# Kernel optimization log

Hardware: AMD Instinct MI355X
Metric: run time of the kernel (lower is better)

The kernel has to match this reference:

```python
import jax, jax.numpy as jnp
import numpy as np

D_MODEL = 1024
N_HEADS = 16
THRESHOLD = 0.8


def setup_inputs() -> dict:
    key = jax.random.key(0)
    ks = jax.random.split(key, 12)
    B, L, D = 2, 2048, D_MODEL
    s = 1.0 / np.sqrt(D)
    return {
        "q_x": jax.random.normal(ks[0], (B, L, D), jnp.float32),
        "k_x": jax.random.normal(ks[1], (B, L, D), jnp.float32),
        "v_x": jax.random.normal(ks[2], (B, L, D), jnp.float32),
        "energy": jax.random.normal(ks[3], (B, L, D), jnp.float32),
        "Wq": jax.random.normal(ks[4], (D, D), jnp.float32) * s,
        "bq": jnp.zeros((D,), jnp.float32),
        "Wk": jax.random.normal(ks[5], (D, D), jnp.float32) * s,
        "bk": jnp.zeros((D,), jnp.float32),
        "Wv": jax.random.normal(ks[6], (D, D), jnp.float32) * s,
        "bv": jnp.zeros((D,), jnp.float32),
        "Wo": jax.random.normal(ks[7], (D, D), jnp.float32) * s,
        "bo": jnp.zeros((D,), jnp.float32),
    }


def reference(q_x, k_x, v_x, energy, Wq, bq, Wk, bk, Wv, bv, Wo, bo):
    B, L, D = q_x.shape
    H = N_HEADS
    Dh = D // H
    # projections -> (B, H, L, Dh)
    Q = (q_x @ Wq + bq).reshape(B, L, H, Dh).transpose(0, 2, 1, 3)
    K = (k_x @ Wk + bk).reshape(B, -1, H, Dh).transpose(0, 2, 1, 3)
    V = (v_x @ Wv + bv).reshape(B, -1, H, Dh).transpose(0, 2, 1, 3)
    sc = jnp.einsum("bhqd,bhkd->bhqk", Q, K) / jnp.sqrt(jnp.float32(Dh))
    # energy mask: (B, Lk) -> broadcast over heads/queries
    mask = jnp.mean(jnp.abs(energy), axis=-1) > THRESHOLD  # (B, Lk)
    sc = jnp.where(mask[:, None, None, :], sc, -jnp.inf)
    w = jnp.nan_to_num(jax.nn.softmax(sc, axis=-1), nan=0.0)
    o = jnp.einsum("bhqk,bhkd->bhqd", w, V).transpose(0, 2, 1, 3).reshape(B, L, D)
    return o @ Wo + bo
```

## Files before the change

### kernel.cpp

```cpp
#include <hip/hip_runtime.h>
#include <hip/hip_bf16.h>
#include <cstdint>

#define DEVI static __device__ __forceinline__

typedef __attribute__((ext_vector_type(8))) short s16x8;
typedef __attribute__((ext_vector_type(4))) float f32x4;
typedef __attribute__((ext_vector_type(2))) unsigned int u32x2;

DEVI unsigned short f2bf(float f) {
  union { float f; unsigned int u; } v; v.f = f;
  return (unsigned short)((v.u + 0x7FFFu + ((v.u >> 16) & 1u)) >> 16);
}

DEVI unsigned int pk2bf(float a, float b) {
  __hip_bfloat162 h2 = __float22bfloat162_rn(float2{a, b});
  return *(unsigned int*)&h2;
}

DEVI void g2l16(const void* g, void* l) {
  __builtin_amdgcn_global_load_lds((const __attribute__((address_space(1))) void*)g,
                                   (__attribute__((address_space(3))) void*)l, 16, 0, 0);
}

__global__ __launch_bounds__(256) void prep_kernel(const float* __restrict__ a,
                                                   const float* __restrict__ b,
                                                   const float* __restrict__ c,
                                                   const float* __restrict__ energy,
                                                   unsigned short* __restrict__ oa,
                                                   unsigned short* __restrict__ ob,
                                                   unsigned short* __restrict__ oc,
                                                   int* __restrict__ flags,
                                                   const float* __restrict__ W0,
                                                   const float* __restrict__ W1,
                                                   const float* __restrict__ W2,
                                                   const float* __restrict__ W3,
                                                   unsigned short* __restrict__ T0,
                                                   unsigned short* __restrict__ T1,
                                                   unsigned short* __restrict__ T2,
                                                   unsigned short* __restrict__ T3) {
  const int gid = blockIdx.x;
  const int t = threadIdx.x;
  __shared__ float lds[64][65];
  if (gid < 6144) {
    const float* in = gid < 2048 ? a : gid < 4096 ? b : c;
    unsigned short* out = gid < 2048 ? oa : gid < 4096 ? ob : oc;
    const int blk = gid & 2047;
    int i = (blk * 256 + t) * 8;
    f32x4 x = *(const f32x4*)(in + i);
    f32x4 y = *(const f32x4*)(in + i + 4);
    s16x8 o;
    o[0] = (short)f2bf(x[0]); o[1] = (short)f2bf(x[1]);
    o[2] = (short)f2bf(x[2]); o[3] = (short)f2bf(x[3]);
    o[4] = (short)f2bf(y[0]); o[5] = (short)f2bf(y[1]);
    o[6] = (short)f2bf(y[2]); o[7] = (short)f2bf(y[3]);
    *(s16x8*)(out + i) = o;
    return;
  }
  if (gid < 10240) {
    const int row = gid - 6144;
    f32x4 v = *(const f32x4*)(energy + (size_t)row * 1024 + t * 4);
    float s = fabsf(v[0]) + fabsf(v[1]) + fabsf(v[2]) + fabsf(v[3]);
#pragma unroll
    for (int off = 1; off < 64; off <<= 1) s += __shfl_xor(s, off);
    if ((t & 63) == 0) lds[0][t >> 6] = s;
    __syncthreads();
    if (t == 0) {
      float tot = lds[0][0] + lds[0][1] + lds[0][2] + lds[0][3];
      flags[row] = (tot * (1.0f / 1024.0f) > 0.8f) ? 1 : 0;
    }
    return;
  }
  const int x = gid - 10240;
  const int z = x >> 8, rem = x & 255;
  const float* W = z == 0 ? W0 : z == 1 ? W1 : z == 2 ? W2 : W3;
  unsigned short* WT = z == 0 ? T0 : z == 1 ? T1 : z == 2 ? T2 : T3;
  const int n0 = (rem >> 4) * 64, k0 = (rem & 15) * 64;
#pragma unroll
  for (int p = 0; p < 4; p++) {
    int r = p * 16 + (t >> 4);
    int cc = (t & 15) * 4;
    f32x4 v = *(const f32x4*)(W + (size_t)(k0 + r) * 1024 + n0 + cc);
    lds[r][cc] = v[0]; lds[r][cc + 1] = v[1]; lds[r][cc + 2] = v[2]; lds[r][cc + 3] = v[3];
  }
  __syncthreads();
  const int cc = t >> 2, gk = t & 3;
#pragma unroll
  for (int hv = 0; hv < 2; hv++) {
    s16x8 o;
#pragma unroll
    for (int j = 0; j < 8; j++) o[j] = (short)f2bf(lds[gk * 16 + hv * 8 + j][cc]);
    *(s16x8*)(WT + (size_t)(n0 + cc) * 1024 + k0 + gk * 16 + hv * 8) = o;
  }
}

__global__ __launch_bounds__(256) void scan_kernel(const int* __restrict__ flags,
                                                   int* __restrict__ inv,
                                                   int* __restrict__ cnt) {
  const int b = blockIdx.x, t = threadIdx.x;
  const int* f = flags + b * 2048;
  int* iv = inv + b * 2048;
#pragma unroll
  for (int j = 0; j < 8; j++) iv[t * 8 + j] = 0;
  int loc[8], s = 0;
#pragma unroll
  for (int j = 0; j < 8; j++) { loc[j] = f[t * 8 + j]; s += loc[j]; }
  const int lane = t & 63, w = t >> 6;
  int ps = s;
#pragma unroll
  for (int off = 1; off < 64; off <<= 1) {
    int o = __shfl_up(ps, off);
    if (lane >= off) ps += o;
  }
  __shared__ int wsum[4];
  if (lane == 63) wsum[w] = ps;
  __syncthreads();
  int woff = 0;
  for (int i = 0; i < w; i++) woff += wsum[i];
  int excl = woff + ps - s;
#pragma unroll
  for (int j = 0; j < 8; j++) {
    if (loc[j]) { iv[excl] = t * 8 + j; excl++; }
  }
  if (t == 255) cnt[b] = woff + ps;
}


__global__ __launch_bounds__(256, 8) void proj_qkv(const unsigned short* __restrict__ xq,
                                                   const unsigned short* __restrict__ xk,
                                                   const unsigned short* __restrict__ xv,
                                                   const unsigned short* __restrict__ WTq,
                                                   const unsigned short* __restrict__ WTk,
                                                   const unsigned short* __restrict__ WTv,
                                                   const float* __restrict__ bq,
                                                   const float* __restrict__ bk,
                                                   const float* __restrict__ bv,
                                                   unsigned short* __restrict__ Qb,
                                                   unsigned short* __restrict__ Kc,
                                                   unsigned short* __restrict__ VTc,
                                                   const int* __restrict__ inv,
                                                   const int* __restrict__ cnt,
                                                   float qsc) {
  const int z = blockIdx.z;
  const int m0 = blockIdx.x * 64;
  const int n0 = blockIdx.y * 64;
  const int b = m0 >> 11;
  const int lc0 = m0 & 2047;
  const int cb = (z == 0) ? 2048 : cnt[b];
  if (lc0 >= cb) return;

  const unsigned short* A  = z == 0 ? xq : z == 1 ? xk : xv;
  const unsigned short* BT = z == 0 ? WTq : z == 1 ? WTk : WTv;
  const float* bias        = z == 0 ? bq : z == 1 ? bk : bv;

  const int t = threadIdx.x;
  const int w = t >> 6, lane = t & 63;
  const int wr = w >> 1, wc = w & 1;
  const int lr = lane & 15, lg = lane >> 4;
  const int sr = lane >> 3, sg = lane & 7;

  int srow[2];
#pragma unroll
  for (int i = 0; i < 2; i++) {
    int r = (i * 4 + w) * 8 + sr;
    srow[i] = (z == 0) ? (m0 + r) : (b * 2048 + inv[b * 2048 + lc0 + r]);
  }

  __shared__ __align__(16) unsigned short As[64 * 64];
  __shared__ __align__(16) unsigned short Bs[64 * 64];

  f32x4 acc[2][2] = {};

  for (int kt = 0; kt < 1024; kt += 64) {
#pragma unroll
    for (int i = 0; i < 2; i++) {
      int r = (i * 4 + w) * 8 + sr;
      g2l16(A + (size_t)srow[i] * 1024 + kt + (sg ^ (r & 7)) * 8,
            (char*)As + (i * 4 + w) * 1024);
      g2l16(BT + (size_t)(n0 + r) * 1024 + kt + (sg ^ (r & 7)) * 8,
            (char*)Bs + (i * 4 + w) * 1024);
    }
    __syncthreads();
#pragma unroll
    for (int ks = 0; ks < 2; ks++) {
      s16x8 af[2], bf[2];
#pragma unroll
      for (int mi = 0; mi < 2; mi++) {
        int row = wr * 32 + mi * 16 + lr;
        af[mi] = *(const s16x8*)((const char*)As + row * 128 + (((ks * 4 + lg) ^ (row & 7)) * 16));
      }
#pragma unroll
      for (int nj = 0; nj < 2; nj++) {
        int row = wc * 32 + nj * 16 + lr;
        bf[nj] = *(const s16x8*)((const char*)Bs + row * 128 + (((ks * 4 + lg) ^ (row & 7)) * 16));
      }
#pragma unroll
      for (int mi = 0; mi < 2; mi++)
#pragma unroll
        for (int nj = 0; nj < 2; nj++)
          acc[mi][nj] = __builtin_amdgcn_mfma_f32_16x16x32_bf16(af[mi], bf[nj], acc[mi][nj], 0, 0, 0);
    }
    __syncthreads();
  }

  float bv2[2];
#pragma unroll
  for (int nj = 0; nj < 2; nj++) bv2[nj] = bias[n0 + wc * 32 + nj * 16 + lr];

#pragma unroll
  for (int mi = 0; mi < 2; mi++) {
    const int mloc = wr * 32 + mi * 16 + lg * 4;
#pragma unroll
    for (int nj = 0; nj < 2; nj++) {
      const int n = n0 + wc * 32 + nj * 16 + lr;
      if (z == 0) {
#pragma unroll
        for (int rg = 0; rg < 4; rg++)
          Qb[(size_t)(m0 + mloc + rg) * 1024 + n] = f2bf((acc[mi][nj][rg] + bv2[nj]) * qsc);
      } else if (z == 1) {
        const int h = n >> 6, dh = n & 63;
#pragma unroll
        for (int rg = 0; rg < 4; rg++) {
          int lc = lc0 + mloc + rg;
          if (lc < cb)
            Kc[((size_t)(b * 16 + h) * 2048 + lc) * 64 + dh] = f2bf(acc[mi][nj][rg] + bv2[nj]);
        }
      } else {
        const int h = n >> 6, dh = n & 63;
#pragma unroll
        for (int rg = 0; rg < 4; rg++) {
          int lc = lc0 + mloc + rg;
          if (lc < cb)
            VTc[((size_t)(b * 16 + h) * 64 + dh) * 2048 + lc] = f2bf(acc[mi][nj][rg] + bv2[nj]);
        }
      }
    }
  }
}

__global__ __launch_bounds__(256, 8) void gemm_out(const unsigned short* __restrict__ A,
                                                   const unsigned short* __restrict__ BT,
                                                   const float* __restrict__ bias,
                                                   float* __restrict__ out) {
  const int m0 = blockIdx.x * 64;
  const int n0 = blockIdx.y * 64;
  const int t = threadIdx.x;
  const int w = t >> 6, lane = t & 63;
  const int wr = w >> 1, wc = w & 1;
  const int lr = lane & 15, lg = lane >> 4;
  const int sr = lane >> 3, sg = lane & 7;

  __shared__ __align__(16) unsigned short As[64 * 64];
  __shared__ __align__(16) unsigned short Bs[64 * 64];

  f32x4 acc[2][2] = {};

  for (int kt = 0; kt < 1024; kt += 64) {
#pragma unroll
    for (int i = 0; i < 2; i++) {
      int r = (i * 4 + w) * 8 + sr;
      g2l16(A + (size_t)(m0 + r) * 1024 + kt + (sg ^ (r & 7)) * 8,
            (char*)As + (i * 4 + w) * 1024);
      g2l16(BT + (size_t)(n0 + r) * 1024 + kt + (sg ^ (r & 7)) * 8,
            (char*)Bs + (i * 4 + w) * 1024);
    }
    __syncthreads();
#pragma unroll
    for (int ks = 0; ks < 2; ks++) {
      s16x8 af[2], bf[2];
#pragma unroll
      for (int mi = 0; mi < 2; mi++) {
        int row = wr * 32 + mi * 16 + lr;
        af[mi] = *(const s16x8*)((const char*)As + row * 128 + (((ks * 4 + lg) ^ (row & 7)) * 16));
      }
#pragma unroll
      for (int nj = 0; nj < 2; nj++) {
        int row = wc * 32 + nj * 16 + lr;
        bf[nj] = *(const s16x8*)((const char*)Bs + row * 128 + (((ks * 4 + lg) ^ (row & 7)) * 16));
      }
#pragma unroll
      for (int mi = 0; mi < 2; mi++)
#pragma unroll
        for (int nj = 0; nj < 2; nj++)
          acc[mi][nj] = __builtin_amdgcn_mfma_f32_16x16x32_bf16(af[mi], bf[nj], acc[mi][nj], 0, 0, 0);
    }
    __syncthreads();
  }

  float bv2[2];
#pragma unroll
  for (int nj = 0; nj < 2; nj++) bv2[nj] = bias[n0 + wc * 32 + nj * 16 + lr];

#pragma unroll
  for (int mi = 0; mi < 2; mi++) {
    const int mb = m0 + wr * 32 + mi * 16 + lg * 4;
#pragma unroll
    for (int nj = 0; nj < 2; nj++) {
      const int n = n0 + wc * 32 + nj * 16 + lr;
#pragma unroll
      for (int rg = 0; rg < 4; rg++)
        out[(size_t)(mb + rg) * 1024 + n] = acc[mi][nj][rg] + bv2[nj];
    }
  }
}

__global__ __launch_bounds__(256) void attn_kernel(const unsigned short* __restrict__ Q,
                                                   const unsigned short* __restrict__ Kc,
                                                   const unsigned short* __restrict__ VTc,
                                                   const int* __restrict__ cnt,
                                                   unsigned short* __restrict__ O) {
  const int bh = blockIdx.x;
  const int qb = blockIdx.y;
  const int b = bh >> 4, h = bh & 15;
  const int t = threadIdx.x, w = t >> 6, lane = t & 63;
  const int lr = lane & 15, lg = lane >> 4;

  __shared__ __align__(16) unsigned short Ks[64 * 64];
  __shared__ __align__(16) unsigned short Vs[64 * 64];
  __shared__ __align__(16) unsigned short Ps[4][16 * 64];

  const size_t bh_off = (size_t)bh * 2048 * 64;
  const int q0 = qb * 64 + w * 16;
  const int cb = cnt[b];
  const int nkb = (cb + 63) >> 6;

  s16x8 qf[2];
#pragma unroll
  for (int ks = 0; ks < 2; ks++)
    qf[ks] = *(const s16x8*)(Q + ((size_t)(b * 2048 + q0 + lr)) * 1024 + h * 64 + ks * 32 + lg * 8);

  f32x4 oacc[4] = {};
  float lsum = 0.f;

  const int sr = lane >> 3, sg = lane & 7;
  for (int kb = 0; kb < nkb; kb++) {
#pragma unroll
    for (int i = 0; i < 2; i++) {
      int r = (i * 4 + w) * 8 + sr;
      g2l16(Kc + bh_off + (size_t)(kb * 64 + r) * 64 + (sg ^ (r & 7)) * 8,
            (char*)Ks + (i * 4 + w) * 1024);
    }
#pragma unroll
    for (int i = 0; i < 2; i++) {
      int r = (i * 4 + w) * 8 + sr;
      g2l16(VTc + bh_off + (size_t)r * 2048 + kb * 64 + (sg ^ (r & 7)) * 8,
            (char*)Vs + (i * 4 + w) * 1024);
    }
    __syncthreads();

    float p[4][4];
    __builtin_amdgcn_s_setprio(1);
#pragma unroll
    for (int t4 = 0; t4 < 4; t4++) {
      f32x4 s = {};
#pragma unroll
      for (int ks = 0; ks < 2; ks++) {
        int row = t4 * 16 + lr;
        s16x8 kf = *(const s16x8*)((const char*)Ks + row * 128 + (((ks * 4 + lg) ^ (row & 7)) * 16));
        s = __builtin_amdgcn_mfma_f32_16x16x32_bf16(kf, qf[ks], s, 0, 0, 0);
      }
      p[t4][0] = s[0]; p[t4][1] = s[1]; p[t4][2] = s[2]; p[t4][3] = s[3];
    }
    __builtin_amdgcn_s_setprio(0);

    if ((kb + 1) * 64 <= cb) {
#pragma unroll
      for (int t4 = 0; t4 < 4; t4++)
#pragma unroll
        for (int rg = 0; rg < 4; rg++) {
          float e = __builtin_amdgcn_exp2f(p[t4][rg]);
          p[t4][rg] = e;
          lsum += e;
        }
    } else {
      const int kbase = kb * 64 + lg * 4;
#pragma unroll
      for (int t4 = 0; t4 < 4; t4++)
#pragma unroll
        for (int rg = 0; rg < 4; rg++) {
          float e = __builtin_amdgcn_exp2f(p[t4][rg]);
          e = (kbase + t4 * 16 + rg < cb) ? e : 0.f;
          p[t4][rg] = e;
          lsum += e;
        }
    }

#pragma unroll
    for (int t4 = 0; t4 < 4; t4++) {
      u32x2 pw = {pk2bf(p[t4][0], p[t4][1]), pk2bf(p[t4][2], p[t4][3])};
      int byte = lr * 128 + ((t4 * 32 + lg * 8) ^ ((lr & 7) << 4));
      *(u32x2*)((char*)Ps + w * 2048 + byte) = pw;
    }

    __builtin_amdgcn_s_setprio(1);
#pragma unroll
    for (int ks = 0; ks < 2; ks++) {
      int byteA = lr * 128 + ((ks * 64 + lg * 16) ^ ((lr & 7) << 4));
      s16x8 af = *(const s16x8*)((const char*)Ps + w * 2048 + byteA);
#pragma unroll
      for (int dt = 0; dt < 4; dt++) {
        int row = dt * 16 + lr;
        s16x8 vf = *(const s16x8*)((const char*)Vs + row * 128 + (((ks * 4 + lg) ^ (row & 7)) * 16));
        oacc[dt] = __builtin_amdgcn_mfma_f32_16x16x32_bf16(af, vf, oacc[dt], 0, 0, 0);
      }
    }
    __builtin_amdgcn_s_setprio(0);
    __syncthreads();
  }

  lsum += __shfl_xor(lsum, 16);
  lsum += __shfl_xor(lsum, 32);

  float rinv[4];
#pragma unroll
  for (int rg = 0; rg < 4; rg++) {
    float ls = __shfl(lsum, lg * 4 + rg);
    rinv[rg] = (ls > 0.f) ? 1.0f / ls : 0.f;
  }
#pragma unroll
  for (int dt = 0; dt < 4; dt++)
#pragma unroll
    for (int rg = 0; rg < 4; rg++) {
      int q = q0 + lg * 4 + rg;
      int d = dt * 16 + lr;
      O[((size_t)(b * 2048 + q)) * 1024 + h * 64 + d] = f2bf(oacc[dt][rg] * rinv[rg]);
    }
}

extern "C" void kernel_launch(void* const* d_in, const int* in_sizes, int n_in,
                              void* d_out, int out_size, void* d_ws, size_t ws_size,
                              hipStream_t stream) {
  (void)in_sizes; (void)n_in; (void)out_size; (void)ws_size;
  const float* q_x = (const float*)d_in[0];
  const float* k_x = (const float*)d_in[1];
  const float* v_x = (const float*)d_in[2];
  const float* energy = (const float*)d_in[3];
  const float* Wq = (const float*)d_in[4];
  const float* bq = (const float*)d_in[5];
  const float* Wk = (const float*)d_in[6];
  const float* bk = (const float*)d_in[7];
  const float* Wv = (const float*)d_in[8];
  const float* bv = (const float*)d_in[9];
  const float* Wo = (const float*)d_in[10];
  const float* bo = (const float*)d_in[11];

  char* ws = (char*)d_ws;
  const size_t MB = 1024 * 1024;
  unsigned short* xq  = (unsigned short*)(ws + 0);
  unsigned short* xk  = (unsigned short*)(ws + 8 * MB);
  unsigned short* xv  = (unsigned short*)(ws + 16 * MB);
  unsigned short* WTq = (unsigned short*)(ws + 24 * MB);
  unsigned short* WTk = (unsigned short*)(ws + 26 * MB);
  unsigned short* WTv = (unsigned short*)(ws + 28 * MB);
  unsigned short* WTo = (unsigned short*)(ws + 30 * MB);
  unsigned short* Qb  = (unsigned short*)(ws + 32 * MB);
  unsigned short* Kc  = (unsigned short*)(ws + 40 * MB);
  unsigned short* VTc = (unsigned short*)(ws + 48 * MB);
  int* flags          = (int*)(ws + 56 * MB);
  int* inv            = (int*)(ws + 56 * MB + 16 * 1024);
  int* cnt            = (int*)(ws + 56 * MB + 32 * 1024);
  unsigned short* Ob  = xq;

  const float QSC = 0.18033688011112042f;

  prep_kernel<<<11264, 256, 0, stream>>>(q_x, k_x, v_x, energy, xq, xk, xv, flags,
                                         Wq, Wk, Wv, Wo, WTq, WTk, WTv, WTo);
  scan_kernel<<<2, 256, 0, stream>>>(flags, inv, cnt);

  proj_qkv<<<dim3(64, 16, 3), 256, 0, stream>>>(xq, xk, xv, WTq, WTk, WTv, bq, bk, bv,
                                                Qb, Kc, VTc, inv, cnt, QSC);

  attn_kernel<<<dim3(32, 32), 256, 0, stream>>>(Qb, Kc, VTc, cnt, Ob);

  gemm_out<<<dim3(64, 16), 256, 0, stream>>>(Ob, WTo, bo, (float*)d_out);
}
```

Measured before the change: 109.3 us.

## Convert only masked K/V rows after scan, compacted; enlarge output GEMM tile

The K and V bf16 conversion moves out of the first prep kernel into a new kernel that runs after the scan. It converts only rows whose energy mask is set and writes them compacted, so the projection GEMM reads contiguous rows instead of gathering through the index array. This cuts fp32 reads and bf16 writes for masked-out rows, at the cost of one more kernel launch. Separately, the output GEMM tile grows from 64x64 to 128x64 for more reuse per block, which halves the block count and removes the occupancy hint.

Result: no change. 108.1 us (-1.1%).

```diff
diff --git a/kernel.cpp b/kernel.cpp
--- a/kernel.cpp
+++ b/kernel.cpp
@@ -23,42 +23,35 @@
                                    (__attribute__((address_space(3))) void*)l, 16, 0, 0);
 }
 
-__global__ __launch_bounds__(256) void prep_kernel(const float* __restrict__ a,
-                                                   const float* __restrict__ b,
-                                                   const float* __restrict__ c,
-                                                   const float* __restrict__ energy,
-                                                   unsigned short* __restrict__ oa,
-                                                   unsigned short* __restrict__ ob,
-                                                   unsigned short* __restrict__ oc,
-                                                   int* __restrict__ flags,
-                                                   const float* __restrict__ W0,
-                                                   const float* __restrict__ W1,
-                                                   const float* __restrict__ W2,
-                                                   const float* __restrict__ W3,
-                                                   unsigned short* __restrict__ T0,
-                                                   unsigned short* __restrict__ T1,
-                                                   unsigned short* __restrict__ T2,
-                                                   unsigned short* __restrict__ T3) {
+__global__ __launch_bounds__(256) void prep1_kernel(const float* __restrict__ q_x,
+                                                    const float* __restrict__ energy,
+                                                    unsigned short* __restrict__ xq,
+                                                    int* __restrict__ flags,
+                                                    const float* __restrict__ W0,
+                                                    const float* __restrict__ W1,
+                                                    const float* __restrict__ W2,
+                                                    const float* __restrict__ W3,
+                                                    unsigned short* __restrict__ T0,
+                                                    unsigned short* __restrict__ T1,
+                                                    unsigned short* __restrict__ T2,
+                                                    unsigned short* __restrict__ T3) {
   const int gid = blockIdx.x;
   const int t = threadIdx.x;
   __shared__ float lds[64][65];
-  if (gid < 6144) {
-    const float* in = gid < 2048 ? a : gid < 4096 ? b : c;
-    unsigned short* out = gid < 2048 ? oa : gid < 4096 ? ob : oc;
-    const int blk = gid & 2047;
-    int i = (blk * 256 + t) * 8;
-    f32x4 x = *(const f32x4*)(in + i);
-    f32x4 y = *(const f32x4*)(in + i + 4);
+  if (gid < 2048) {
+    int i = (gid * 256 + t) * 8;
+    f32x4 x = *(const f32x4*)(q_x + i);
+    f32x4 y = *(const f32x4*)(q_x + i + 4);
     s16x8 o;
     o[0] = (short)f2bf(x[0]); o[1] = (short)f2bf(x[1]);
     o[2] = (short)f2bf(x[2]); o[3] = (short)f2bf(x[3]);
     o[4] = (short)f2bf(y[0]); o[5] = (short)f2bf(y[1]);
     o[6] = (short)f2bf(y[2]); o[7] = (short)f2bf(y[3]);
-    *(s16x8*)(out + i) = o;
+    *(s16x8*)(xq + i) = o;
     return;
   }
-  if (gid < 10240) {
-    const int row = gid - 6144;
+  if (gid < 6144) {
+    const int row = gid - 2048;
     f32x4 v = *(const f32x4*)(energy + (size_t)row * 1024 + t * 4);
     float s = fabsf(v[0]) + fabsf(v[1]) + fabsf(v[2]) + fabsf(v[3]);
 #pragma unroll
@@ -71,7 +64,7 @@
     }
     return;
   }
-  const int x = gid - 10240;
+  const int x = gid - 6144;
   const int z = x >> 8, rem = x & 255;
   const float* W = z == 0 ? W0 : z == 1 ? W1 : z == 2 ? W2 : W3;
   unsigned short* WT = z == 0 ? T0 : z == 1 ? T1 : z == 2 ? T2 : T3;
@@ -125,10 +118,40 @@
   if (t == 255) cnt[b] = woff + ps;
 }
 
+__global__ __launch_bounds__(256) void prep2_kernel(const float* __restrict__ k_x,
+                                                    const float* __restrict__ v_x,
+                                                    const int* __restrict__ inv,
+                                                    const int* __restrict__ cnt,
+                                                    unsigned short* __restrict__ xkc,
+                                                    unsigned short* __restrict__ xvc) {
+  const int gid = blockIdx.x;
+  const int t = threadIdx.x;
+  const int isv = gid >> 11;
+  const int lid = gid & 2047;
+  const int b = lid >> 10;
+  const int cp = (lid & 1023) * 2;
+  const int cb = cnt[b];
+  if (cp >= cb) return;
+  const float* in = isv ? v_x : k_x;
+  unsigned short* out = isv ? xvc : xkc;
+  const int rowc = cp + (t >> 7);
+  if (rowc >= cb) return;
+  const int src = inv[b * 2048 + rowc];
+  const int col = (t & 127) * 8;
+  const float* ip = in + ((size_t)(b * 2048 + src)) * 1024 + col;
+  f32x4 x = *(const f32x4*)ip;
+  f32x4 y = *(const f32x4*)(ip + 4);
+  s16x8 o;
+  o[0] = (short)f2bf(x[0]); o[1] = (short)f2bf(x[1]);
+  o[2] = (short)f2bf(x[2]); o[3] = (short)f2bf(x[3]);
+  o[4] = (short)f2bf(y[0]); o[5] = (short)f2bf(y[1]);
+  o[6] = (short)f2bf(y[2]); o[7] = (short)f2bf(y[3]);
+  *(s16x8*)(out + ((size_t)(b * 2048 + rowc)) * 1024 + col) = o;
+}
 
 __global__ __launch_bounds__(256, 8) void proj_qkv(const unsigned short* __restrict__ xq,
-                                                   const unsigned short* __restrict__ xk,
-                                                   const unsigned short* __restrict__ xv,
+                                                   const unsigned short* __restrict__ xkc,
+                                                   const unsigned short* __restrict__ xvc,
                                                    const unsigned short* __restrict__ WTq,
                                                    const unsigned short* __restrict__ WTk,
                                                    const unsigned short* __restrict__ WTv,
@@ -138,7 +161,6 @@
                                                    unsigned short* __restrict__ Qb,
                                                    unsigned short* __restrict__ Kc,
                                                    unsigned short* __restrict__ VTc,
-                                                   const int* __restrict__ inv,
                                                    const int* __restrict__ cnt,
                                                    float qsc) {
   const int z = blockIdx.z;
@@ -149,7 +171,7 @@
   const int cb = (z == 0) ? 2048 : cnt[b];
   if (lc0 >= cb) return;
 
-  const unsigned short* A  = z == 0 ? xq : z == 1 ? xk : xv;
+  const unsigned short* A  = z == 0 ? xq : z == 1 ? xkc : xvc;
   const unsigned short* BT = z == 0 ? WTq : z == 1 ? WTk : WTv;
   const float* bias        = z == 0 ? bq : z == 1 ? bk : bv;
 
@@ -159,13 +181,6 @@
   const int lr = lane & 15, lg = lane >> 4;
   const int sr = lane >> 3, sg = lane & 7;
 
-  int srow[2];
-#pragma unroll
-  for (int i = 0; i < 2; i++) {
-    int r = (i * 4 + w) * 8 + sr;
-    srow[i] = (z == 0) ? (m0 + r) : (b * 2048 + inv[b * 2048 + lc0 + r]);
-  }
-
   __shared__ __align__(16) unsigned short As[64 * 64];
   __shared__ __align__(16) unsigned short Bs[64 * 64];
 
@@ -175,7 +190,7 @@
 #pragma unroll
     for (int i = 0; i < 2; i++) {
       int r = (i * 4 + w) * 8 + sr;
-      g2l16(A + (size_t)srow[i] * 1024 + kt + (sg ^ (r & 7)) * 8,
+      g2l16(A + (size_t)(m0 + r) * 1024 + kt + (sg ^ (r & 7)) * 8,
             (char*)As + (i * 4 + w) * 1024);
       g2l16(BT + (size_t)(n0 + r) * 1024 + kt + (sg ^ (r & 7)) * 8,
             (char*)Bs + (i * 4 + w) * 1024);
@@ -238,11 +253,11 @@
   }
 }
 
-__global__ __launch_bounds__(256, 8) void gemm_out(const unsigned short* __restrict__ A,
-                                                   const unsigned short* __restrict__ BT,
-                                                   const float* __restrict__ bias,
-                                                   float* __restrict__ out) {
-  const int m0 = blockIdx.x * 64;
+__global__ __launch_bounds__(256) void gemm_out(const unsigned short* __restrict__ A,
+                                                const unsigned short* __restrict__ BT,
+                                                const float* __restrict__ bias,
+                                                float* __restrict__ out) {
+  const int m0 = blockIdx.x * 128;
   const int n0 = blockIdx.y * 64;
   const int t = threadIdx.x;
   const int w = t >> 6, lane = t & 63;
@@ -250,27 +265,31 @@
   const int lr = lane & 15, lg = lane >> 4;
   const int sr = lane >> 3, sg = lane & 7;
 
-  __shared__ __align__(16) unsigned short As[64 * 64];
+  __shared__ __align__(16) unsigned short As[128 * 64];
   __shared__ __align__(16) unsigned short Bs[64 * 64];
 
-  f32x4 acc[2][2] = {};
+  f32x4 acc[4][2] = {};
 
   for (int kt = 0; kt < 1024; kt += 64) {
 #pragma unroll
-    for (int i = 0; i < 2; i++) {
+    for (int i = 0; i < 4; i++) {
       int r = (i * 4 + w) * 8 + sr;
       g2l16(A + (size_t)(m0 + r) * 1024 + kt + (sg ^ (r & 7)) * 8,
             (char*)As + (i * 4 + w) * 1024);
+    }
+#pragma unroll
+    for (int i = 0; i < 2; i++) {
+      int r = (i * 4 + w) * 8 + sr;
       g2l16(BT + (size_t)(n0 + r) * 1024 + kt + (sg ^ (r & 7)) * 8,
             (char*)Bs + (i * 4 + w) * 1024);
     }
     __syncthreads();
 #pragma unroll
     for (int ks = 0; ks < 2; ks++) {
-      s16x8 af[2], bf[2];
-#pragma unroll
-      for (int mi = 0; mi < 2; mi++) {
-        int row = wr * 32 + mi * 16 + lr;
+      s16x8 af[4], bf[2];
+#pragma unroll
+      for (int mi = 0; mi < 4; mi++) {
+        int row = wr * 64 + mi * 16 + lr;
         af[mi] = *(const s16x8*)((const char*)As + row * 128 + (((ks * 4 + lg) ^ (row & 7)) * 16));
       }
 #pragma unroll
@@ -279,7 +298,7 @@
         bf[nj] = *(const s16x8*)((const char*)Bs + row * 128 + (((ks * 4 + lg) ^ (row & 7)) * 16));
       }
 #pragma unroll
-      for (int mi = 0; mi < 2; mi++)
+      for (int mi = 0; mi < 4; mi++)
 #pragma unroll
         for (int nj = 0; nj < 2; nj++)
           acc[mi][nj] = __builtin_amdgcn_mfma_f32_16x16x32_bf16(af[mi], bf[nj], acc[mi][nj], 0, 0, 0);
@@ -292,8 +311,8 @@
   for (int nj = 0; nj < 2; nj++) bv2[nj] = bias[n0 + wc * 32 + nj * 16 + lr];
 
 #pragma unroll
-  for (int mi = 0; mi < 2; mi++) {
-    const int mb = m0 + wr * 32 + mi * 16 + lg * 4;
+  for (int mi = 0; mi < 4; mi++) {
+    const int mb = m0 + wr * 64 + mi * 16 + lg * 4;
 #pragma unroll
     for (int nj = 0; nj < 2; nj++) {
       const int n = n0 + wc * 32 + nj * 16 + lr;
@@ -447,8 +466,8 @@
   char* ws = (char*)d_ws;
   const size_t MB = 1024 * 1024;
   unsigned short* xq  = (unsigned short*)(ws + 0);
-  unsigned short* xk  = (unsigned short*)(ws + 8 * MB);
-  unsigned short* xv  = (unsigned short*)(ws + 16 * MB);
+  unsigned short* xkc = (unsigned short*)(ws + 8 * MB);
+  unsigned short* xvc = (unsigned short*)(ws + 16 * MB);
   unsigned short* WTq = (unsigned short*)(ws + 24 * MB);
   unsigned short* WTk = (unsigned short*)(ws + 26 * MB);
   unsigned short* WTv = (unsigned short*)(ws + 28 * MB);
@@ -463,14 +482,15 @@
 
   const float QSC = 0.18033688011112042f;
 
-  prep_kernel<<<11264, 256, 0, stream>>>(q_x, k_x, v_x, energy, xq, xk, xv, flags,
+  prep1_kernel<<<7168, 256, 0, stream>>>(q_x, energy, xq, flags,
                                          Wq, Wk, Wv, Wo, WTq, WTk, WTv, WTo);
   scan_kernel<<<2, 256, 0, stream>>>(flags, inv, cnt);
-
-  proj_qkv<<<dim3(64, 16, 3), 256, 0, stream>>>(xq, xk, xv, WTq, WTk, WTv, bq, bk, bv,
-                                                Qb, Kc, VTc, inv, cnt, QSC);
+  prep2_kernel<<<4096, 256, 0, stream>>>(k_x, v_x, inv, cnt, xkc, xvc);
+
+  proj_qkv<<<dim3(64, 16, 3), 256, 0, stream>>>(xq, xkc, xvc, WTq, WTk, WTv, bq, bk, bv,
+                                                Qb, Kc, VTc, cnt, QSC);
 
   attn_kernel<<<dim3(32, 32), 256, 0, stream>>>(Qb, Kc, VTc, cnt, Ob);
 
-  gemm_out<<<dim3(64, 16), 256, 0, stream>>>(Ob, WTo, bo, (float*)d_out);
-}
+  gemm_out<<<dim3(32, 16), 256, 0, stream>>>(Ob, WTo, bo, (float*)d_out);
+}
```
